# Performance work log

Hardware: AMD Instinct MI355X
Metric: run time of the kernel (lower is better)

The kernel has to match this reference:

```python
import jax, jax.numpy as jnp
import numpy as np

KERNEL_MUL = 2.0
KERNEL_NUM = 5


def setup_inputs() -> dict:
    key = jax.random.key(0)
    k1, k2 = jax.random.split(key)
    source = jax.random.normal(k1, (4096, 256), dtype=jnp.float32)
    target = jax.random.normal(k2, (4096, 256), dtype=jnp.float32)
    return {"source": source, "target": target}


def _mmd(source, target):
    n = source.shape[0]
    m = target.shape[0]
    ns = n + m
    total = jnp.concatenate([source, target], axis=0)  # [ns, D]
    # Pairwise squared L2 distances without the O(ns^2 * D) broadcast tensor:
    # ||x_i - x_j||^2 = ||x_i||^2 + ||x_j||^2 - 2 <x_i, x_j>
    sq = jnp.sum(total * total, axis=1)  # [ns]
    l2 = sq[:, None] + sq[None, :] - 2.0 * (total @ total.T)  # [ns, ns]
    # bandwidth computed on detached data in the original (L2_distance.data)
    bandwidth = jax.lax.stop_gradient(jnp.sum(l2)) / (ns * ns - ns)
    bandwidth = bandwidth / (KERNEL_MUL ** (KERNEL_NUM // 2))
    # multi-bandwidth Gaussian kernel sum (fused single pass over l2)
    kernels = jnp.zeros_like(l2)
    for i in range(KERNEL_NUM):
        kernels = kernels + jnp.exp(-l2 / (bandwidth * KERNEL_MUL ** i))
    xx = jnp.sum(kernels[:n, :n]) / (n * n)
    xy = jnp.sum(kernels[:n, n:]) / (-n * m)
    yx = jnp.sum(kernels[n:, :n]) / (-m * n)
    yy = jnp.sum(kernels[n:, n:]) / (m * m)
    return xx + xy + yx + yy


def reference(source, target):
    return _mmd(source, target)
```

## Files before the change

### kernel.cpp

```cpp
#include <hip/hip_runtime.h>
#include <hip/hip_bf16.h>
#include <stdint.h>

#define NS 8192
#define NHALF 4096
#define DIM 256
#define BLK 128
#define BK 32
#define NKT (DIM / BK)
#define NTILES (NS / BLK)
#define HALF_TILES (NHALF / BLK)
#define NTRI (NTILES * (NTILES + 1) / 2)
#define PREP_BLOCKS 256

typedef __attribute__((ext_vector_type(8))) short bf16x8;
typedef __attribute__((ext_vector_type(4))) float f32x4;
typedef __attribute__((ext_vector_type(8))) unsigned short u16x8;

#define XB_OFF   0
#define SQ_OFF   (NS * DIM * 2)
#define PART_OFF (SQ_OFF + NS * 4)
#define ACC_OFF  (PART_OFF + PREP_BLOCKS * DIM * 4)
#define C0_OFF   (ACC_OFF + 8)
#define WS_NEED  (C0_OFF + 16)

__device__ __forceinline__ unsigned short f2bf(float f) {
  unsigned int u = __float_as_uint(f);
  u += 0x7fffu + ((u >> 16) & 1u);
  return (unsigned short)(u >> 16);
}
__device__ __forceinline__ float bf2f(unsigned short h) {
  return __uint_as_float(((unsigned int)h) << 16);
}

__global__ __launch_bounds__(256) void mmd_prep(
    const float* __restrict__ src, const float* __restrict__ tgt,
    unsigned short* __restrict__ Xb, float* __restrict__ sq,
    float* __restrict__ partials) {
  int tid = threadIdx.x;
  int lane32 = tid & 31;
  int rgrp = tid >> 5;
  int c = lane32 * 8;
  int rowBase = blockIdx.x * 32;

  float colpart[8];
#pragma unroll
  for (int j = 0; j < 8; ++j) colpart[j] = 0.f;

#pragma unroll
  for (int p = 0; p < 4; ++p) {
    int row = rowBase + p * 8 + rgrp;
    const float* X = (row < NHALF) ? (src + (size_t)row * DIM)
                                   : (tgt + (size_t)(row - NHALF) * DIM);
    float4 v0 = *(const float4*)(X + c);
    float4 v1 = *(const float4*)(X + c + 4);
    float vals[8] = {v0.x, v0.y, v0.z, v0.w, v1.x, v1.y, v1.z, v1.w};
    u16x8 h;
    float s = 0.f;
#pragma unroll
    for (int j = 0; j < 8; ++j) {
      unsigned short b = f2bf(vals[j]);
      h[j] = b;
      float rb = bf2f(b);
      s += rb * rb;
      colpart[j] += rb;
    }
    *(u16x8*)(Xb + (size_t)row * DIM + c) = h;
    for (int o = 16; o > 0; o >>= 1) s += __shfl_down(s, o, 32);
    if (lane32 == 0) sq[row] = s;
  }

  __shared__ float cp[8][DIM];
  *(float4*)&cp[rgrp][c]     = make_float4(colpart[0], colpart[1], colpart[2], colpart[3]);
  *(float4*)&cp[rgrp][c + 4] = make_float4(colpart[4], colpart[5], colpart[6], colpart[7]);
  __syncthreads();
  float s8 = 0.f;
#pragma unroll
  for (int r = 0; r < 8; ++r) s8 += cp[r][tid];
  partials[blockIdx.x * DIM + tid] = s8;
}

__global__ __launch_bounds__(256) void mmd_band(
    const float* __restrict__ partials, const float* __restrict__ sq,
    float* __restrict__ c0out) {
  __shared__ double buf2[DIM];
  __shared__ float buf1[DIM];
  int tid = threadIdx.x;
  float cs = 0.f;
  for (int b = 0; b < PREP_BLOCKS; ++b) cs += partials[b * DIM + tid];
  float s1 = 0.f;
  for (int k = 0; k < NS / DIM; ++k) s1 += sq[k * DIM + tid];
  buf2[tid] = (double)cs * (double)cs;
  buf1[tid] = s1;
  __syncthreads();
  for (int o = 128; o > 0; o >>= 1) {
    if (tid < o) { buf2[tid] += buf2[tid + o]; buf1[tid] += buf1[tid + o]; }
    __syncthreads();
  }
  if (tid == 0) {
    double S1 = (double)buf1[0];
    double S2 = buf2[0];
    double sum_l2 = 2.0 * (double)NS * S1 - 2.0 * S2;
    double bw = sum_l2 / ((double)NS * (double)NS - (double)NS);
    bw = bw / 4.0;
    c0out[0] = (float)(1.4426950408889634 / bw);
  }
}

#define STAGE(KT, BUF)                                                        \
  {                                                                           \
    _Pragma("unroll") for (int it = 0; it < 2; ++it) {                        \
      int idx = it * 256 + tid;                         \
      int r = idx >> 2, g = idx & 3;          \
      int gs = g ^ ((r >> 1) & 3);          \
      const unsigned short* ga =                                              \
          Xb + (size_t)(rowBase + r) * DIM + (KT)*BK + gs * 8;                \
      __builtin_amdgcn_global_load_lds(                                       \
          (const __attribute__((address_space(1))) void*)ga,                  \
          (__attribute__((address_space(3))) void*)(&As[BUF][idx * 8]), 16,   \
          0, 0);                                                              \
      const unsigned short* gb =                                              \
          Xb + (size_t)(colBase + r) * DIM + (KT)*BK + gs * 8;                \
      __builtin_amdgcn_global_load_lds(                                       \
          (const __attribute__((address_space(1))) void*)gb,                  \
          (__attribute__((address_space(3))) void*)(&Bs[BUF][idx * 8]), 16,   \
          0, 0);                                                              \
    }                                                                         \
  }

__global__ __launch_bounds__(256, 2) void mmd_gram(
    const unsigned short* __restrict__ Xb, const float* __restrict__ sq,
    const float* __restrict__ c0p, double* __restrict__ accK) {
  int l = blockIdx.x;
  int bj = (int)((sqrtf(8.f * (float)l + 1.f) - 1.f) * 0.5f);
  while ((bj + 1) * (bj + 2) / 2 <= l) bj++;
  while (bj * (bj + 1) / 2 > l) bj--;
  int bi = l - bj * (bj + 1) / 2;

  __shared__ __align__(16) unsigned short As[2][BLK * BK];
  __shared__ __align__(16) unsigned short Bs[2][BLK * BK];
  int tid = threadIdx.x;
  int wave = tid >> 6;
  int lane = tid & 63;
  int rowBase = bi * BLK, colBase = bj * BLK;
  int wr = (wave >> 1) * 64;
  int wc = (wave & 1) * 64;

  float c0v = *c0p;
  float sqr[4][4], sqc[4];
  int r4 = (lane >> 4) * 4;
#pragma unroll
  for (int m = 0; m < 4; ++m)
#pragma unroll
    for (int r = 0; r < 4; ++r)
      sqr[m][r] = sq[rowBase + wr + m * 16 + r4 + r];
#pragma unroll
  for (int n = 0; n < 4; ++n)
    sqc[n] = sq[colBase + wc + n * 16 + (lane & 15)];

  f32x4 acc[4][4];
#pragma unroll
  for (int m = 0; m < 4; ++m)
#pragma unroll
    for (int n = 0; n < 4; ++n) acc[m][n] = (f32x4){0.f, 0.f, 0.f, 0.f};

  STAGE(0, 0);
  STAGE(1, 1);

#pragma unroll
  for (int kt = 0; kt < NKT; ++kt) {
    int cur = kt & 1;
    if (kt == NKT - 1)
      asm volatile("s_waitcnt vmcnt(0)" ::: "memory");
    else
      asm volatile("s_waitcnt vmcnt(4)" ::: "memory");
    __builtin_amdgcn_s_barrier();

    bf16x8 af[4], bfr[4];
    int kg = lane >> 4;
#pragma unroll
    for (int m = 0; m < 4; ++m) {
      int r = wr + m * 16 + (lane & 15);
      af[m] = *(const bf16x8*)(&As[cur][r * BK + (kg ^ ((r >> 1) & 3)) * 8]);
    }
#pragma unroll
    for (int n = 0; n < 4; ++n) {
      int r = wc + n * 16 + (lane & 15);
      bfr[n] = *(const bf16x8*)(&Bs[cur][r * BK + (kg ^ ((r >> 1) & 3)) * 8]);
    }
    asm volatile("s_waitcnt lgkmcnt(0)" ::: "memory");
    __builtin_amdgcn_sched_barrier(0);
    __builtin_amdgcn_s_barrier();

    if (kt < NKT - 2) STAGE(kt + 2, cur);

#pragma unroll
    for (int m = 0; m < 4; ++m)
#pragma unroll
      for (int n = 0; n < 4; ++n)
        acc[m][n] = __builtin_amdgcn_mfma_f32_16x16x32_bf16(
            af[m], bfr[n], acc[m][n], 0, 0, 0);
  }

  float cE = -0.0625f * c0v;
  float t2 = -2.f * cE;
  float a_[4][4], b_[4];
#pragma unroll
  for (int m = 0; m < 4; ++m)
#pragma unroll
    for (int r = 0; r < 4; ++r) a_[m][r] = cE * sqr[m][r];
#pragma unroll
  for (int n = 0; n < 4; ++n) b_[n] = cE * sqc[n];

  float tsum = 0.f;
#pragma unroll
  for (int m = 0; m < 4; ++m)
#pragma unroll
    for (int n = 0; n < 4; ++n)
#pragma unroll
      for (int r = 0; r < 4; ++r) {
        float arg = fmaf(acc[m][n][r], t2, a_[m][r] + b_[n]);
        float e4 = exp2f(arg);
        float e3 = e4 * e4;
        float e2 = e3 * e3;
        float e1 = e2 * e2;
        float e0 = e1 * e1;
        tsum += ((e4 + e3) + (e2 + e1)) + e0;
      }

  float* red4 = (float*)&As[0][0];
#pragma unroll
  for (int o = 32; o > 0; o >>= 1) tsum += __shfl_down(tsum, o);
  if (lane == 0) red4[wave] = tsum;
  __syncthreads();
  if (tid == 0) {
    float t = (red4[0] + red4[1]) + (red4[2] + red4[3]);
    float sign = ((bi < HALF_TILES) == (bj < HALF_TILES)) ? 1.f : -1.f;
    float factor = (bi == bj) ? sign : 2.f * sign;
    atomicAdd(accK, (double)(factor * t));
  }
}

__global__ void mmd_final(const double* __restrict__ accK, float* __restrict__ out) {
  out[0] = (float)(accK[0] / ((double)NHALF * (double)NHALF));
}

extern "C" void kernel_launch(void* const* d_in, const int* in_sizes, int n_in,
                              void* d_out, int out_size, void* d_ws, size_t ws_size,
                              hipStream_t stream) {
  if (ws_size < (size_t)WS_NEED) return;
  const float* src = (const float*)d_in[0];
  const float* tgt = (const float*)d_in[1];
  char* ws = (char*)d_ws;
  unsigned short* Xb = (unsigned short*)(ws + XB_OFF);
  float* sq          = (float*)(ws + SQ_OFF);
  float* partials    = (float*)(ws + PART_OFF);
  double* accK       = (double*)(ws + ACC_OFF);
  float* c0          = (float*)(ws + C0_OFF);

  hipMemsetAsync(ws + ACC_OFF, 0, 16, stream);
  mmd_prep<<<PREP_BLOCKS, 256, 0, stream>>>(src, tgt, Xb, sq, partials);
  mmd_band<<<1, 256, 0, stream>>>(partials, sq, c0);
  mmd_gram<<<NTRI, 256, 0, stream>>>(Xb, sq, c0, accK);
  mmd_final<<<1, 1, 0, stream>>>(accK, (float*)d_out);
}
```

Before: 68.22 us.

## Process strips of up to four row tiles per block, reusing column tile

Each gram block now walks up to four row tiles against a fixed column tile, so there are 544 strips in place of 2080 single-tile blocks. The next tile's first K slices and its squared norms are prefetched during the current tile's MMA loop. The accumulator memset is folded into the prep kernel, and the bandwidth reduction kernel now uses 1024 threads. This cuts launch and tail overhead and per-block setup, but the column tile is still reloaded each iteration, and fewer, longer blocks may leave CUs unevenly loaded.

```diff
diff --git a/kernel.cpp b/kernel.cpp
--- a/kernel.cpp
+++ b/kernel.cpp
@@ -10,7 +10,7 @@
 #define NKT (DIM / BK)
 #define NTILES (NS / BLK)
 #define HALF_TILES (NHALF / BLK)
-#define NTRI (NTILES * (NTILES + 1) / 2)
+#define NSTRIPS 544
 #define PREP_BLOCKS 256
 
 typedef __attribute__((ext_vector_type(8))) short bf16x8;
@@ -36,8 +36,9 @@
 __global__ __launch_bounds__(256) void mmd_prep(
     const float* __restrict__ src, const float* __restrict__ tgt,
     unsigned short* __restrict__ Xb, float* __restrict__ sq,
-    float* __restrict__ partials) {
+    float* __restrict__ partials, double* __restrict__ accK) {
   int tid = threadIdx.x;
+  if (blockIdx.x == 0 && tid == 0) accK[0] = 0.0;
   int lane32 = tid & 31;
   int rgrp = tid >> 5;
   int c = lane32 * 8;
@@ -80,26 +81,35 @@
   partials[blockIdx.x * DIM + tid] = s8;
 }
 
-__global__ __launch_bounds__(256) void mmd_band(
+__global__ __launch_bounds__(1024) void mmd_band(
     const float* __restrict__ partials, const float* __restrict__ sq,
     float* __restrict__ c0out) {
-  __shared__ double buf2[DIM];
-  __shared__ float buf1[DIM];
+  __shared__ float CS[4][DIM];
+  __shared__ float L1[1024];
+  __shared__ double D2[DIM];
   int tid = threadIdx.x;
+  int q = tid >> 8, col = tid & 255;
   float cs = 0.f;
-  for (int b = 0; b < PREP_BLOCKS; ++b) cs += partials[b * DIM + tid];
-  float s1 = 0.f;
-  for (int k = 0; k < NS / DIM; ++k) s1 += sq[k * DIM + tid];
-  buf2[tid] = (double)cs * (double)cs;
-  buf1[tid] = s1;
+  for (int b = 0; b < PREP_BLOCKS / 4; ++b)
+    cs += partials[(q * 64 + b) * DIM + col];
+  CS[q][col] = cs;
+  const float4* s4 = (const float4*)sq;
+  float4 va = s4[tid * 2], vb = s4[tid * 2 + 1];
+  L1[tid] = (va.x + va.y + va.z + va.w) + (vb.x + vb.y + vb.z + vb.w);
+  __syncthreads();
+  if (tid < DIM) {
+    float ctot = (CS[0][tid] + CS[1][tid]) + (CS[2][tid] + CS[3][tid]);
+    D2[tid] = (double)ctot * (double)ctot;
+    L1[tid] = (L1[tid] + L1[tid + 256]) + (L1[tid + 512] + L1[tid + 768]);
+  }
   __syncthreads();
   for (int o = 128; o > 0; o >>= 1) {
-    if (tid < o) { buf2[tid] += buf2[tid + o]; buf1[tid] += buf1[tid + o]; }
+    if (tid < o) { D2[tid] += D2[tid + o]; L1[tid] += L1[tid + o]; }
     __syncthreads();
   }
   if (tid == 0) {
-    double S1 = (double)buf1[0];
-    double S2 = buf2[0];
+    double S1 = (double)L1[0];
+    double S2 = D2[0];
     double sum_l2 = 2.0 * (double)NS * S1 - 2.0 * S2;
     double bw = sum_l2 / ((double)NS * (double)NS - (double)NS);
     bw = bw / 4.0;
@@ -107,14 +117,14 @@
   }
 }
 
-#define STAGE(KT, BUF)                                                        \
+#define STAGE(RB, KT, BUF)                                                    \
   {                                                                           \
     _Pragma("unroll") for (int it = 0; it < 2; ++it) {                        \
       int idx = it * 256 + tid;                         \
       int r = idx >> 2, g = idx & 3;          \
       int gs = g ^ ((r >> 1) & 3);          \
       const unsigned short* ga =                                              \
-          Xb + (size_t)(rowBase + r) * DIM + (KT)*BK + gs * 8;                \
+          Xb + (size_t)((RB) + r) * DIM + (KT)*BK + gs * 8;                   \
       __builtin_amdgcn_global_load_lds(                                       \
           (const __attribute__((address_space(1))) void*)ga,                  \
           (__attribute__((address_space(3))) void*)(&As[BUF][idx * 8]), 16,   \
@@ -131,102 +141,128 @@
 __global__ __launch_bounds__(256, 2) void mmd_gram(
     const unsigned short* __restrict__ Xb, const float* __restrict__ sq,
     const float* __restrict__ c0p, double* __restrict__ accK) {
-  int l = blockIdx.x;
-  int bj = (int)((sqrtf(8.f * (float)l + 1.f) - 1.f) * 0.5f);
-  while ((bj + 1) * (bj + 2) / 2 <= l) bj++;
-  while (bj * (bj + 1) / 2 > l) bj--;
-  int bi = l - bj * (bj + 1) / 2;
+  int S = blockIdx.x;
+  int m0 = (int)sqrtf((float)S * 0.5f);
+  if (m0 > 16) m0 = 16;
+  int bj = 4 * m0;
+  int C = 2 * m0 * (m0 + 1);
+  while (C > S) { bj--; C -= (bj >> 2) + 1; }
+  while (C + ((bj >> 2) + 1) <= S) { C += (bj >> 2) + 1; bj++; }
+  int sIdx = S - C;
+  int bi0 = 4 * sIdx;
+  int T = bj - bi0 + 1; if (T > 4) T = 4;
 
   __shared__ __align__(16) unsigned short As[2][BLK * BK];
   __shared__ __align__(16) unsigned short Bs[2][BLK * BK];
   int tid = threadIdx.x;
   int wave = tid >> 6;
   int lane = tid & 63;
-  int rowBase = bi * BLK, colBase = bj * BLK;
+  int colBase = bj * BLK;
   int wr = (wave >> 1) * 64;
   int wc = (wave & 1) * 64;
 
   float c0v = *c0p;
-  float sqr[4][4], sqc[4];
   int r4 = (lane >> 4) * 4;
+  f32x4 sqrC[4], sqrN[4];
 #pragma unroll
   for (int m = 0; m < 4; ++m)
-#pragma unroll
-    for (int r = 0; r < 4; ++r)
-      sqr[m][r] = sq[rowBase + wr + m * 16 + r4 + r];
-#pragma unroll
-  for (int n = 0; n < 4; ++n)
-    sqc[n] = sq[colBase + wc + n * 16 + (lane & 15)];
-
-  f32x4 acc[4][4];
-#pragma unroll
-  for (int m = 0; m < 4; ++m)
-#pragma unroll
-    for (int n = 0; n < 4; ++n) acc[m][n] = (f32x4){0.f, 0.f, 0.f, 0.f};
-
-  STAGE(0, 0);
-  STAGE(1, 1);
-
-#pragma unroll
-  for (int kt = 0; kt < NKT; ++kt) {
-    int cur = kt & 1;
-    if (kt == NKT - 1)
-      asm volatile("s_waitcnt vmcnt(0)" ::: "memory");
-    else
-      asm volatile("s_waitcnt vmcnt(4)" ::: "memory");
-    __builtin_amdgcn_s_barrier();
-
-    bf16x8 af[4], bfr[4];
-    int kg = lane >> 4;
-#pragma unroll
-    for (int m = 0; m < 4; ++m) {
-      int r = wr + m * 16 + (lane & 15);
-      af[m] = *(const bf16x8*)(&As[cur][r * BK + (kg ^ ((r >> 1) & 3)) * 8]);
-    }
-#pragma unroll
-    for (int n = 0; n < 4; ++n) {
-      int r = wc + n * 16 + (lane & 15);
-      bfr[n] = *(const bf16x8*)(&Bs[cur][r * BK + (kg ^ ((r >> 1) & 3)) * 8]);
-    }
-    asm volatile("s_waitcnt lgkmcnt(0)" ::: "memory");
-    __builtin_amdgcn_sched_barrier(0);
-    __builtin_amdgcn_s_barrier();
-
-    if (kt < NKT - 2) STAGE(kt + 2, cur);
-
-#pragma unroll
-    for (int m = 0; m < 4; ++m)
-#pragma unroll
-      for (int n = 0; n < 4; ++n)
-        acc[m][n] = __builtin_amdgcn_mfma_f32_16x16x32_bf16(
-            af[m], bfr[n], acc[m][n], 0, 0, 0);
-  }
+    sqrC[m] = *(const f32x4*)&sq[bi0 * BLK + wr + m * 16 + r4];
+  float sqc[4];
+#pragma unroll
+  for (int n = 0; n < 4; ++n) sqc[n] = sq[colBase + wc + n * 16 + (lane & 15)];
 
   float cE = -0.0625f * c0v;
   float t2 = -2.f * cE;
-  float a_[4][4], b_[4];
-#pragma unroll
-  for (int m = 0; m < 4; ++m)
-#pragma unroll
-    for (int r = 0; r < 4; ++r) a_[m][r] = cE * sqr[m][r];
+  float b_[4];
 #pragma unroll
   for (int n = 0; n < 4; ++n) b_[n] = cE * sqc[n];
 
+  f32x4 acc[4][4];
   float tsum = 0.f;
-#pragma unroll
-  for (int m = 0; m < 4; ++m)
-#pragma unroll
-    for (int n = 0; n < 4; ++n)
-#pragma unroll
-      for (int r = 0; r < 4; ++r) {
-        float arg = fmaf(acc[m][n][r], t2, a_[m][r] + b_[n]);
-        float e4 = exp2f(arg);
-        float e3 = e4 * e4;
-        float e2 = e3 * e3;
-        float e1 = e2 * e2;
-        float e0 = e1 * e1;
-        tsum += ((e4 + e3) + (e2 + e1)) + e0;
-      }
+
+  STAGE(bi0 * BLK, 0, 0);
+  STAGE(bi0 * BLK, 1, 1);
+
+  for (int t = 0; t < T; ++t) {
+    int rowBase = (bi0 + t) * BLK;
+    int rowBaseN = rowBase + BLK;
+    bool hasNext = (t + 1 < T);
+#pragma unroll
+    for (int m = 0; m < 4; ++m)
+#pragma unroll
+      for (int n = 0; n < 4; ++n) acc[m][n] = (f32x4){0.f, 0.f, 0.f, 0.f};
+
+#pragma unroll
+    for (int kt = 0; kt < NKT; ++kt) {
+      if (kt == NKT - 1 && t == T - 1)
+        asm volatile("s_waitcnt vmcnt(0)" ::: "memory");
+      else
+        asm volatile("s_waitcnt vmcnt(4)" ::: "memory");
+      __builtin_amdgcn_s_barrier();
+
+      bf16x8 af[4], bfr[4];
+      int cur = kt & 1;
+      int kg = lane >> 4;
+#pragma unroll
+      for (int m = 0; m < 4; ++m) {
+        int r = wr + m * 16 + (lane & 15);
+        af[m] = *(const bf16x8*)(&As[cur][r * BK + (kg ^ ((r >> 1) & 3)) * 8]);
+      }
+#pragma unroll
+      for (int n = 0; n < 4; ++n) {
+        int r = wc + n * 16 + (lane & 15);
+        bfr[n] = *(const bf16x8*)(&Bs[cur][r * BK + (kg ^ ((r >> 1) & 3)) * 8]);
+      }
+      asm volatile("s_waitcnt lgkmcnt(0)" ::: "memory");
+      __builtin_amdgcn_sched_barrier(0);
+      __builtin_amdgcn_s_barrier();
+
+      if (kt == 1 && hasNext) {
+#pragma unroll
+        for (int m = 0; m < 4; ++m)
+          sqrN[m] = *(const f32x4*)&sq[rowBaseN + wr + m * 16 + r4];
+      }
+      if (kt <= 5) { STAGE(rowBase, kt + 2, cur); }
+      else if (hasNext) {
+        if (kt == 6) { STAGE(rowBaseN, 0, 0); }
+        else         { STAGE(rowBaseN, 1, 1); }
+      }
+
+#pragma unroll
+      for (int m = 0; m < 4; ++m)
+#pragma unroll
+        for (int n = 0; n < 4; ++n)
+          acc[m][n] = __builtin_amdgcn_mfma_f32_16x16x32_bf16(
+              af[m], bfr[n], acc[m][n], 0, 0, 0);
+    }
+
+    int bi = bi0 + t;
+    float a_[4][4];
+#pragma unroll
+    for (int m = 0; m < 4; ++m)
+#pragma unroll
+      for (int r = 0; r < 4; ++r) a_[m][r] = cE * sqrC[m][r];
+    float part = 0.f;
+#pragma unroll
+    for (int m = 0; m < 4; ++m)
+#pragma unroll
+      for (int n = 0; n < 4; ++n)
+#pragma unroll
+        for (int r = 0; r < 4; ++r) {
+          float arg = fmaf(acc[m][n][r], t2, a_[m][r] + b_[n]);
+          float e4 = exp2f(arg);
+          float e3 = e4 * e4;
+          float e2 = e3 * e3;
+          float e1 = e2 * e2;
+          float e0 = e1 * e1;
+          part += ((e4 + e3) + (e2 + e1)) + e0;
+        }
+    float sign = ((bi < HALF_TILES) == (bj < HALF_TILES)) ? 1.f : -1.f;
+    float factor = (bi == bj) ? sign : 2.f * sign;
+    tsum = fmaf(factor, part, tsum);
+#pragma unroll
+    for (int m = 0; m < 4; ++m) sqrC[m] = sqrN[m];
+  }
 
   float* red4 = (float*)&As[0][0];
 #pragma unroll
@@ -234,10 +270,8 @@
   if (lane == 0) red4[wave] = tsum;
   __syncthreads();
   if (tid == 0) {
-    float t = (red4[0] + red4[1]) + (red4[2] + red4[3]);
-    float sign = ((bi < HALF_TILES) == (bj < HALF_TILES)) ? 1.f : -1.f;
-    float factor = (bi == bj) ? sign : 2.f * sign;
-    atomicAdd(accK, (double)(factor * t));
+    float tt = (red4[0] + red4[1]) + (red4[2] + red4[3]);
+    atomicAdd(accK, (double)tt);
   }
 }
 
@@ -258,9 +292,8 @@
   double* accK       = (double*)(ws + ACC_OFF);
   float* c0          = (float*)(ws + C0_OFF);
 
-  hipMemsetAsync(ws + ACC_OFF, 0, 16, stream);
-  mmd_prep<<<PREP_BLOCKS, 256, 0, stream>>>(src, tgt, Xb, sq, partials);
-  mmd_band<<<1, 256, 0, stream>>>(partials, sq, c0);
-  mmd_gram<<<NTRI, 256, 0, stream>>>(Xb, sq, c0, accK);
+  mmd_prep<<<PREP_BLOCKS, 256, 0, stream>>>(src, tgt, Xb, sq, partials, accK);
+  mmd_band<<<1, 1024, 0, stream>>>(partials, sq, c0);
+  mmd_gram<<<NSTRIPS, 256, 0, stream>>>(Xb, sq, c0, accK);
   mmd_final<<<1, 1, 0, stream>>>(accK, (float*)d_out);
 }
```

Result: faster. 66.80 us (-2.1%).
